# Performance work log

Measured on AMD Instinct MI355X. Metric: run time of the kernel, lower is better.

The kernel has to match this reference:

```python
import math
import jax, jax.numpy as jnp
import numpy as np

B, S, D, H = 4, 2048, 768, 8


def setup_inputs() -> dict:
    key = jax.random.key(0)
    ks = jax.random.split(key, 8)
    x = jax.random.normal(ks[0], (B, S, D), dtype=jnp.float32)
    # padding mask: True = masked position, shape [B, S, 1] as consumed by forward
    attention_mask = jax.random.randint(ks[1], (B, S, 1), 0, 2) == 1
    W_q = jax.random.normal(ks[2], (D, D), dtype=jnp.float32) * 0.02
    b_q = jax.random.normal(ks[3], (D,), dtype=jnp.float32) * 0.02
    W_v = jax.random.normal(ks[4], (D, D), dtype=jnp.float32) * 0.02
    b_v = jax.random.normal(ks[5], (D,), dtype=jnp.float32) * 0.02
    gamma = jnp.ones((D,), dtype=jnp.float32)
    beta = jnp.zeros((D,), dtype=jnp.float32)
    return {"x": x, "attention_mask": attention_mask, "W_q": W_q, "b_q": b_q,
            "W_v": W_v, "b_v": b_v, "gamma": gamma, "beta": beta}


def reference(x, attention_mask, W_q, b_q, W_v, b_v, gamma, beta):
    b, s, d = x.shape
    dk = d // H
    scale = math.sqrt(dk)
    q = (x @ W_q.T + b_q).reshape(b, s, H, dk).transpose(0, 2, 1, 3)  # [B,H,S,dk]
    # faithful to source: k and v BOTH use the V projection (original bug)
    kv = (x @ W_v.T + b_v).reshape(b, s, H, dk).transpose(0, 2, 1, 3)
    k = kv
    v = kv
    weight = jnp.einsum('bhid,bhjd->bhij', q, k) / scale  # [B,H,S,S]
    pad = attention_mask[:, None, :, :]                   # [B,1,S,1] -> broadcast over heads, j
    causal = jnp.triu(jnp.ones((s, s), dtype=bool), 1)    # [S,S]
    mask = pad | causal
    weight = jnp.where(mask, jnp.float32(-1e9), weight)
    # faithful: softmax over dim=2 (the query axis), as in the source
    score = jax.nn.softmax(weight, axis=2)
    out = jnp.einsum('bhij,bhjd->bhid', score, v)         # [B,H,S,dk]
    out = out.transpose(0, 2, 1, 3).reshape(b, s, d)
    out = out + x                                          # residual
    mu = jnp.mean(out, axis=-1, keepdims=True)
    var = jnp.mean((out - mu) ** 2, axis=-1, keepdims=True)
    return (out - mu) / jnp.sqrt(var + 1e-5) * gamma + beta
```

## Files before the change

### kernel.cpp

```cpp
#include <hip/hip_runtime.h>

#define B 4
#define S 2048
#define D 768
#define H 8
#define DK 96
#define NBH (B*H)
#define SD (B*S*D)

typedef __bf16 bf16x8 __attribute__((ext_vector_type(8)));
typedef float f32x4 __attribute__((ext_vector_type(4)));
typedef unsigned short ushort_t;
typedef __attribute__((ext_vector_type(8))) unsigned short ushort8;
typedef __attribute__((ext_vector_type(4))) unsigned short us4;

static constexpr float NEG = -1.0e9f;
static constexpr float SCALE_L2E = 0.14724515567714155f;

__device__ __forceinline__ float exp2v(float x) { return __builtin_amdgcn_exp2f(x); }

__device__ __forceinline__ ushort_t f2bf(float f) {
    union { float f; unsigned u; } v; v.f = f;
    unsigned r = v.u + 0x7fffu + ((v.u >> 16) & 1u);
    return (ushort_t)(r >> 16);
}

__device__ __forceinline__ unsigned cvt_pk(float a, float b) {
    unsigned d;
    asm("v_cvt_pk_bf16_f32 %0, %1, %2" : "=v"(d) : "v"(a), "v"(b));
    return d;
}
__device__ __forceinline__ ushort8 pack8(const float4& a, const float4& b) {
    union { unsigned u[4]; ushort8 s; } r;
    r.u[0] = cvt_pk(a.x, a.y); r.u[1] = cvt_pk(a.z, a.w);
    r.u[2] = cvt_pk(b.x, b.y); r.u[3] = cvt_pk(b.z, b.w);
    return r.s;
}
__device__ __forceinline__ us4 pack4(const float4& a) {
    union { unsigned u[2]; us4 s; } r;
    r.u[0] = cvt_pk(a.x, a.y); r.u[1] = cvt_pk(a.z, a.w);
    return r.s;
}

#define MFMA16(a, b, c) __builtin_amdgcn_mfma_f32_16x16x32_bf16((a), (b), (c), 0, 0, 0)

__global__ __launch_bounds__(256) void convert_bf16(
    const float* __restrict__ wq, const float* __restrict__ wv,
    ushort_t* __restrict__ wqb, ushort_t* __restrict__ wvb)
{
    const int stride = gridDim.x * 256;
    const int idx = blockIdx.x * 256 + threadIdx.x;
    for (int i = idx; i < (D * D) / 4; i += stride) {
        ((us4*)wqb)[i] = pack4(((const float4*)wq)[i]);
        ((us4*)wvb)[i] = pack4(((const float4*)wv)[i]);
    }
}

__global__ __launch_bounds__(256) void in_proj_gemm(
    const float* __restrict__ x,
    const ushort_t* __restrict__ wqb, const float* __restrict__ bq,
    const ushort_t* __restrict__ wvb, const float* __restrict__ bv,
    ushort_t* __restrict__ Qb, ushort_t* __restrict__ KVb,
    ushort_t* __restrict__ KVt)
{
    const ushort_t* __restrict__ Wm = blockIdx.z ? wvb : wqb;
    const float* __restrict__ bia   = blockIdx.z ? bv : bq;
    ushort_t* __restrict__ outp     = blockIdx.z ? KVb : Qb;
    const float osc = blockIdx.z ? 1.0f : SCALE_L2E;

    const int bn = blockIdx.x * 128;
    const int bm = blockIdx.y * 128;
    const int tid = threadIdx.x;
    const int lane = tid & 63;
    const int wid = tid >> 6;
    const int wm = (wid >> 1) * 64, wn = (wid & 1) * 64;
    const int lr = lane & 15, lg = lane >> 4;

    __shared__ __align__(16) ushort_t As[2][128][40];
    __shared__ __align__(16) ushort_t Bs[2][128][40];

    const int r0 = tid >> 2, c8 = (tid & 3) * 8;
    const float*    xg0 = &x [(size_t)(bm + r0) * D + c8];
    const float*    xg1 = xg0 + (size_t)64 * D;
    const ushort_t* wg0 = &Wm[(size_t)(bn + r0) * D + c8];
    const ushort_t* wg1 = wg0 + (size_t)64 * D;

    float4 xv[4];
    ushort8 wv2[2];

    f32x4 acc[4][4];
    #pragma unroll
    for (int m = 0; m < 4; ++m)
        #pragma unroll
        for (int n = 0; n < 4; ++n) acc[m][n] = (f32x4){0.f, 0.f, 0.f, 0.f};

    {
        xv[0] = *(const float4*)(xg0);     xv[1] = *(const float4*)(xg0 + 4);
        xv[2] = *(const float4*)(xg1);     xv[3] = *(const float4*)(xg1 + 4);
        wv2[0] = *(const ushort8*)(wg0);   wv2[1] = *(const ushort8*)(wg1);
        *(ushort8*)&As[0][r0][c8]      = pack8(xv[0], xv[1]);
        *(ushort8*)&As[0][r0 + 64][c8] = pack8(xv[2], xv[3]);
        *(ushort8*)&Bs[0][r0][c8]      = wv2[0];
        *(ushort8*)&Bs[0][r0 + 64][c8] = wv2[1];
    }

    for (int k = 0; k < 24; ++k) {
        __syncthreads();
        const int buf = k & 1;
        if (k < 23) {
            const int ko = (k + 1) * 32;
            xv[0] = *(const float4*)(xg0 + ko);     xv[1] = *(const float4*)(xg0 + ko + 4);
            xv[2] = *(const float4*)(xg1 + ko);     xv[3] = *(const float4*)(xg1 + ko + 4);
            wv2[0] = *(const ushort8*)(wg0 + ko);   wv2[1] = *(const ushort8*)(wg1 + ko);
        }
        bf16x8 a[4], bfr[4];
        #pragma unroll
        for (int m = 0; m < 4; ++m) a[m]   = *(const bf16x8*)&As[buf][wm + m * 16 + lr][lg * 8];
        #pragma unroll
        for (int n = 0; n < 4; ++n) bfr[n] = *(const bf16x8*)&Bs[buf][wn + n * 16 + lr][lg * 8];
        #pragma unroll
        for (int m = 0; m < 4; ++m)
            #pragma unroll
            for (int n = 0; n < 4; ++n)
                acc[m][n] = MFMA16(a[m], bfr[n], acc[m][n]);
        if (k < 23) {
            const int nb = (k + 1) & 1;
            *(ushort8*)&As[nb][r0][c8]      = pack8(xv[0], xv[1]);
            *(ushort8*)&As[nb][r0 + 64][c8] = pack8(xv[2], xv[3]);
            *(ushort8*)&Bs[nb][r0][c8]      = wv2[0];
            *(ushort8*)&Bs[nb][r0 + 64][c8] = wv2[1];
        }
    }

    #pragma unroll
    for (int m = 0; m < 4; ++m) {
        #pragma unroll
        for (int n = 0; n < 4; ++n) {
            int col = bn + wn + n * 16 + lr;
            float bb = bia[col];
            int row0 = bm + wm + m * 16 + lg * 4;
            us4 o;
            #pragma unroll
            for (int r = 0; r < 4; ++r) o[r] = f2bf((acc[m][n][r] + bb) * osc);
            #pragma unroll
            for (int r = 0; r < 4; ++r) outp[(size_t)(row0 + r) * D + col] = o[r];
            if (blockIdx.z) {
                int hh = col / DK, dd = col - hh * DK;
                int bb2 = row0 >> 11, ss = row0 & (S - 1);
                *(us4*)&KVt[((size_t)(bb2 * H + hh) * DK + dd) * S + ss] = o;
            }
        }
    }
}

__global__ __launch_bounds__(256) void col_stats(
    const ushort_t* __restrict__ Qb, const ushort_t* __restrict__ KVb,
    const int* __restrict__ amask,
    float* __restrict__ colM, float* __restrict__ colSinv)
{
    const int bh = blockIdx.y;
    const int jt = (blockIdx.x + 8 * ((bh >> 3) & 3)) & 31;
    const int b = bh >> 3, h = bh & 7;
    const int j0 = jt * 64;
    const int tid = threadIdx.x;
    const int lane = tid & 63;
    const int w = tid >> 6;
    const int lr = lane & 15, lg = lane >> 4;

    __shared__ __align__(16) ushort_t qs[2][64][104];
    __shared__ int pads[2][64];

    bf16x8 kf[3];
    #pragma unroll
    for (int ks2 = 0; ks2 < 3; ++ks2)
        kf[ks2] = *(const bf16x8*)&KVb[(size_t)(b * S + j0 + w * 16 + lr) * D + h * DK + ks2 * 32 + lg * 8];

    int kr[3], kc[3];
    const ushort_t* qg[3];
    #pragma unroll
    for (int k3 = 0; k3 < 3; ++k3) {
        int c = tid + k3 * 256;
        kr[k3] = c / 12; kc[k3] = (c % 12) * 8;
        qg[k3] = &Qb[(size_t)(b * S + j0 + kr[k3]) * D + h * DK + kc[k3]];
    }
    const int* pg = amask + b * S + j0 + (tid < 64 ? tid : 0);

    ushort8 pq[3]; int ppad = 0;
    #pragma unroll
    for (int k3 = 0; k3 < 3; ++k3) { pq[k3] = *(const ushort8*)qg[k3]; qg[k3] += (size_t)64 * D; }
    if (tid < 64) { ppad = *pg; }
    pg += 64;

    float m = NEG, ssum = 0.f;
    const int jg = j0 + w * 16 + lr;
    const int nit = (S / 64) - jt;

    for (int t = 0; t < nit; ++t) {
        const int buf = t & 1;
        const int i0 = j0 + t * 64;
        #pragma unroll
        for (int k3 = 0; k3 < 3; ++k3) *(ushort8*)&qs[buf][kr[k3]][kc[k3]] = pq[k3];
        if (tid < 64) pads[buf][tid] = ppad;
        __syncthreads();
        if (t + 1 < nit) {
            #pragma unroll
            for (int k3 = 0; k3 < 3; ++k3) { pq[k3] = *(const ushort8*)qg[k3]; qg[k3] += (size_t)64 * D; }
            if (tid < 64) { ppad = *pg; }
            pg += 64;
        }

        f32x4 dacc[4];
        #pragma unroll
        for (int f = 0; f < 4; ++f) dacc[f] = (f32x4){0.f, 0.f, 0.f, 0.f};
        #pragma unroll
        for (int ks2 = 0; ks2 < 3; ++ks2) {
            #pragma unroll
            for (int f = 0; f < 4; ++f) {
                bf16x8 afr = *(const bf16x8*)&qs[buf][f * 16 + lr][ks2 * 32 + lg * 8];
                dacc[f] = MFMA16(afr, kf[ks2], dacc[f]);
            }
        }

        #pragma unroll
        for (int f = 0; f < 4; ++f) {
            const int ib = f * 16 + lg * 4;
            float wv[4];
            #pragma unroll
            for (int r = 0; r < 4; ++r) {
                int ig = i0 + ib + r;
                wv[r] = (pads[buf][ib + r] != 0 || jg > ig) ? NEG : dacc[f][r];
            }
            float vmax = fmaxf(fmaxf(wv[0], wv[1]), fmaxf(wv[2], wv[3]));
            float mn = fmaxf(m, vmax);
            ssum = ssum * exp2v(m - mn)
                 + exp2v(wv[0] - mn) + exp2v(wv[1] - mn)
                 + exp2v(wv[2] - mn) + exp2v(wv[3] - mn);
            m = mn;
        }
    }

    float m2 = m, s2 = ssum;
    #pragma unroll
    for (int off = 16; off < 64; off <<= 1) {
        float mo = __shfl_xor(m2, off);
        float so = __shfl_xor(s2, off);
        float mn = fmaxf(m2, mo);
        s2 = s2 * exp2v(m2 - mn) + so * exp2v(mo - mn);
        m2 = mn;
    }
    if (lane < 16) {
        if (m2 == NEG) s2 += (float)j0;
        colM[bh * S + jg] = m2;
        colSinv[bh * S + jg] = 1.0f / s2;
    }
}

__global__ __launch_bounds__(256, 4) void attn_pv(
    const ushort_t* __restrict__ Qb, const ushort_t* __restrict__ KVb,
    const ushort_t* __restrict__ KVt,
    const int* __restrict__ amask,
    const float* __restrict__ colM, const float* __restrict__ colSinv,
    const float* __restrict__ x, float* __restrict__ out)
{
    const int bh = blockIdx.y;
    const int it = (blockIdx.x + 8 * ((bh >> 3) & 3)) & 31;
    const int b = bh >> 3, h = bh & 7;
    const int i0 = it * 64;
    const int tid = threadIdx.x;
    const int lane = tid & 63;
    const int w = tid >> 6;
    const int lr = lane & 15, lg = lane >> 4;

    __shared__ __align__(16) ushort_t kvs[64][104];
    __shared__ __align__(16) ushort_t kvt[96][88];
    __shared__ __align__(16) ushort_t ps[64][72];
    __shared__ __align__(16) float cm[64];
    __shared__ __align__(16) float csv[64];

    bf16x8 qf[3];
    #pragma unroll
    for (int ks2 = 0; ks2 < 3; ++ks2)
        qf[ks2] = *(const bf16x8*)&Qb[(size_t)(b * S + i0 + w * 16 + lr) * D + h * DK + ks2 * 32 + lg * 8];

    const int my_pad = (int)(amask[b * S + i0 + w * 16 + lr] != 0);
    const int i_g = i0 + w * 16 + lr;

    int kr[3], kc[3], tr[3], tc[3];
    const ushort_t* kvg[3];
    const ushort_t* ktg[3];
    #pragma unroll
    for (int k3 = 0; k3 < 3; ++k3) {
        int c = tid + k3 * 256;
        kr[k3] = c / 12;  kc[k3] = (c % 12) * 8;
        tr[k3] = c >> 3;  tc[k3] = (c & 7) * 8;
        kvg[k3] = &KVb[(size_t)(b * S + kr[k3]) * D + h * DK + kc[k3]];
        ktg[k3] = &KVt[((size_t)(b * H + h) * DK + tr[k3]) * S + tc[k3]];
    }
    const float* cmg  = colM    + (size_t)bh * S + (tid < 64 ? tid : 0);
    const float* csvg = colSinv + (size_t)bh * S + (tid < 64 ? tid : 0);

    ushort8 pkv[3], pkt[3]; float pcm = 0.f, pcsv = 0.f;
    #pragma unroll
    for (int k3 = 0; k3 < 3; ++k3) {
        pkv[k3] = *(const ushort8*)kvg[k3];  kvg[k3] += (size_t)64 * D;
        pkt[k3] = *(const ushort8*)ktg[k3];  ktg[k3] += 64;
    }
    if (tid < 64) { pcm = *cmg; pcsv = *csvg; }
    cmg += 64; csvg += 64;

    f32x4 acc[6];
    #pragma unroll
    for (int df = 0; df < 6; ++df) acc[df] = (f32x4){0.f, 0.f, 0.f, 0.f};

    for (int jt2 = 0; jt2 <= it; ++jt2) {
        const int j0 = jt2 * 64;
        __syncthreads();
        #pragma unroll
        for (int k3 = 0; k3 < 3; ++k3) {
            *(ushort8*)&kvs[kr[k3]][kc[k3]] = pkv[k3];
            *(ushort8*)&kvt[tr[k3]][tc[k3]] = pkt[k3];
        }
        if (tid < 64) { cm[tid] = pcm; csv[tid] = pcsv; }
        __syncthreads();
        if (jt2 < it) {
            #pragma unroll
            for (int k3 = 0; k3 < 3; ++k3) {
                pkv[k3] = *(const ushort8*)kvg[k3];  kvg[k3] += (size_t)64 * D;
                pkt[k3] = *(const ushort8*)ktg[k3];  ktg[k3] += 64;
            }
            if (tid < 64) { pcm = *cmg; pcsv = *csvg; }
            cmg += 64; csvg += 64;
        }

        f32x4 dacc[4];
        #pragma unroll
        for (int jf = 0; jf < 4; ++jf) dacc[jf] = (f32x4){0.f, 0.f, 0.f, 0.f};
        #pragma unroll
        for (int ks2 = 0; ks2 < 3; ++ks2) {
            #pragma unroll
            for (int jf = 0; jf < 4; ++jf) {
                bf16x8 bfr = *(const bf16x8*)&kvs[jf * 16 + lr][ks2 * 32 + lg * 8];
                dacc[jf] = MFMA16(bfr, qf[ks2], dacc[jf]);
            }
        }

        #pragma unroll
        for (int jf = 0; jf < 4; ++jf) {
            const int jbase = jf * 16 + lg * 4;
            f32x4 cmv  = *(const f32x4*)&cm[jbase];
            f32x4 csvv = *(const f32x4*)&csv[jbase];
            float pv[4];
            #pragma unroll
            for (int r = 0; r < 4; ++r) {
                int jgl = j0 + jbase + r;
                bool msk = my_pad || (jgl > i_g);
                float wvv = msk ? NEG : dacc[jf][r];
                pv[r] = exp2v(wvv - cmv[r]) * csvv[r];
            }
            union { unsigned u[2]; uint2 v; } o;
            o.u[0] = cvt_pk(pv[0], pv[1]);
            o.u[1] = cvt_pk(pv[2], pv[3]);
            *(uint2*)&ps[w * 16 + lr][jbase] = o.v;
        }

        #pragma unroll
        for (int ks2 = 0; ks2 < 2; ++ks2) {
            bf16x8 afr = *(const bf16x8*)&ps[w * 16 + lr][ks2 * 32 + lg * 8];
            #pragma unroll
            for (int df = 0; df < 6; ++df) {
                bf16x8 bfr = *(const bf16x8*)&kvt[df * 16 + lr][ks2 * 32 + lg * 8];
                acc[df] = MFMA16(afr, bfr, acc[df]);
            }
        }
    }

    #pragma unroll
    for (int df = 0; df < 6; ++df) {
        int d = h * DK + df * 16 + lr;
        #pragma unroll
        for (int r = 0; r < 4; ++r) {
            size_t gi = (size_t)(b * S + i0 + w * 16 + lg * 4 + r) * D + d;
            out[gi] = acc[df][r] + x[gi];
        }
    }
}

__global__ __launch_bounds__(256) void layer_norm(
    float* __restrict__ out,
    const float* __restrict__ gamma, const float* __restrict__ beta)
{
    const int row = blockIdx.x * 4 + (threadIdx.x >> 6);
    const int lane = threadIdx.x & 63;
    float* o = out + (size_t)row * D;

    float4 v[3];
    #pragma unroll
    for (int p = 0; p < 3; ++p) v[p] = *(const float4*)&o[lane * 4 + p * 256];

    float s = 0.f;
    #pragma unroll
    for (int p = 0; p < 3; ++p) s += v[p].x + v[p].y + v[p].z + v[p].w;
    #pragma unroll
    for (int off = 1; off < 64; off <<= 1) s += __shfl_xor(s, off);
    const float mu = s * (1.0f / D);

    float q = 0.f;
    #pragma unroll
    for (int p = 0; p < 3; ++p) {
        float a = v[p].x - mu, bb = v[p].y - mu, c = v[p].z - mu, dd = v[p].w - mu;
        q += a * a + bb * bb + c * c + dd * dd;
    }
    #pragma unroll
    for (int off = 1; off < 64; off <<= 1) q += __shfl_xor(q, off);
    const float inv = 1.0f / sqrtf(q * (1.0f / D) + 1e-5f);

    #pragma unroll
    for (int p = 0; p < 3; ++p) {
        float4 g = *(const float4*)&gamma[lane * 4 + p * 256];
        float4 bt = *(const float4*)&beta[lane * 4 + p * 256];
        float4 r;
        r.x = (v[p].x - mu) * inv * g.x + bt.x;
        r.y = (v[p].y - mu) * inv * g.y + bt.y;
        r.z = (v[p].z - mu) * inv * g.z + bt.z;
        r.w = (v[p].w - mu) * inv * g.w + bt.w;
        *(float4*)&o[lane * 4 + p * 256] = r;
    }
}

extern "C" void kernel_launch(void* const* d_in, const int* in_sizes, int n_in,
                              void* d_out, int out_size, void* d_ws, size_t ws_size,
                              hipStream_t stream)
{
    const float* x     = (const float*)d_in[0];
    const int*   amask = (const int*)  d_in[1];
    const float* Wq    = (const float*)d_in[2];
    const float* bq    = (const float*)d_in[3];
    const float* Wv    = (const float*)d_in[4];
    const float* bv    = (const float*)d_in[5];
    const float* gamma = (const float*)d_in[6];
    const float* beta  = (const float*)d_in[7];
    float* out = (float*)d_out;

    ushort_t* wqb  = (ushort_t*)d_ws;
    ushort_t* wvb  = wqb + (size_t)D * D;
    ushort_t* Qb   = wvb + (size_t)D * D;
    ushort_t* KVb  = Qb  + (size_t)SD;
    ushort_t* KVt  = KVb + (size_t)SD;
    float* colM    = (float*)(KVt + (size_t)SD);
    float* colSinv = colM + (size_t)NBH * S;

    convert_bf16<<<576, 256, 0, stream>>>(Wq, Wv, wqb, wvb);
    in_proj_gemm<<<dim3(D / 128, (B * S) / 128, 2), 256, 0, stream>>>(
        x, wqb, bq, wvb, bv, Qb, KVb, KVt);
    col_stats<<<dim3(S / 64, NBH), 256, 0, stream>>>(
        Qb, KVb, amask, colM, colSinv);
    attn_pv<<<dim3(S / 64, NBH), 256, 0, stream>>>(
        Qb, KVb, KVt, amask, colM, colSinv, x, out);
    layer_norm<<<(B * S) / 4, 256, 0, stream>>>(out, gamma, beta);
}
```

Measured before the change: 175.1 us.

## Double per-block tile to 128 rows in col_stats and attn_pv

Both attention kernels now give each block 128 columns or rows instead of 64, with each wave holding two 16-row fragments. Each staged Q or KV tile in shared memory is therefore reused for twice as many MFMAs, halving tile loads and block count. The tile-to-block mapping now reverses order for half the heads to balance causal work. The cost is more registers (launch bounds lowered to 3 waves), half as many blocks (512), and coarser load-balance granularity.

New measurement: 260.6 us. 48.9% more time.

```diff
diff --git a/kernel.cpp b/kernel.cpp
--- a/kernel.cpp
+++ b/kernel.cpp
@@ -153,15 +153,16 @@
     }
 }
 
-__global__ __launch_bounds__(256) void col_stats(
+__global__ __launch_bounds__(256, 3) void col_stats(
     const ushort_t* __restrict__ Qb, const ushort_t* __restrict__ KVb,
     const int* __restrict__ amask,
     float* __restrict__ colM, float* __restrict__ colSinv)
 {
     const int bh = blockIdx.y;
-    const int jt = (blockIdx.x + 8 * ((bh >> 3) & 3)) & 31;
+    const int bxs = blockIdx.x & 15;
+    const int jt = (bh & 16) ? (15 - bxs) : bxs;
     const int b = bh >> 3, h = bh & 7;
-    const int j0 = jt * 64;
+    const int j0 = jt * 128;
     const int tid = threadIdx.x;
     const int lane = tid & 63;
     const int w = tid >> 6;
@@ -170,10 +171,12 @@
     __shared__ __align__(16) ushort_t qs[2][64][104];
     __shared__ int pads[2][64];
 
-    bf16x8 kf[3];
-    #pragma unroll
-    for (int ks2 = 0; ks2 < 3; ++ks2)
-        kf[ks2] = *(const bf16x8*)&KVb[(size_t)(b * S + j0 + w * 16 + lr) * D + h * DK + ks2 * 32 + lg * 8];
+    bf16x8 kf[2][3];
+    #pragma unroll
+    for (int cf = 0; cf < 2; ++cf)
+        #pragma unroll
+        for (int ks2 = 0; ks2 < 3; ++ks2)
+            kf[cf][ks2] = *(const bf16x8*)&KVb[(size_t)(b * S + j0 + w * 32 + cf * 16 + lr) * D + h * DK + ks2 * 32 + lg * 8];
 
     int kr[3], kc[3];
     const ushort_t* qg[3];
@@ -191,9 +194,11 @@
     if (tid < 64) { ppad = *pg; }
     pg += 64;
 
-    float m = NEG, ssum = 0.f;
-    const int jg = j0 + w * 16 + lr;
-    const int nit = (S / 64) - jt;
+    float m[2] = {NEG, NEG}, ssum[2] = {0.f, 0.f};
+    int jg[2];
+    jg[0] = j0 + w * 32 + lr;
+    jg[1] = j0 + w * 32 + 16 + lr;
+    const int nit = 32 - 2 * jt;
 
     for (int t = 0; t < nit; ++t) {
         const int buf = t & 1;
@@ -209,53 +214,62 @@
             pg += 64;
         }
 
-        f32x4 dacc[4];
-        #pragma unroll
-        for (int f = 0; f < 4; ++f) dacc[f] = (f32x4){0.f, 0.f, 0.f, 0.f};
+        f32x4 dacc[2][4];
+        #pragma unroll
+        for (int cf = 0; cf < 2; ++cf)
+            #pragma unroll
+            for (int f = 0; f < 4; ++f) dacc[cf][f] = (f32x4){0.f, 0.f, 0.f, 0.f};
         #pragma unroll
         for (int ks2 = 0; ks2 < 3; ++ks2) {
             #pragma unroll
             for (int f = 0; f < 4; ++f) {
                 bf16x8 afr = *(const bf16x8*)&qs[buf][f * 16 + lr][ks2 * 32 + lg * 8];
-                dacc[f] = MFMA16(afr, kf[ks2], dacc[f]);
-            }
-        }
-
-        #pragma unroll
-        for (int f = 0; f < 4; ++f) {
-            const int ib = f * 16 + lg * 4;
-            float wv[4];
-            #pragma unroll
-            for (int r = 0; r < 4; ++r) {
-                int ig = i0 + ib + r;
-                wv[r] = (pads[buf][ib + r] != 0 || jg > ig) ? NEG : dacc[f][r];
-            }
-            float vmax = fmaxf(fmaxf(wv[0], wv[1]), fmaxf(wv[2], wv[3]));
-            float mn = fmaxf(m, vmax);
-            ssum = ssum * exp2v(m - mn)
-                 + exp2v(wv[0] - mn) + exp2v(wv[1] - mn)
-                 + exp2v(wv[2] - mn) + exp2v(wv[3] - mn);
-            m = mn;
-        }
-    }
-
-    float m2 = m, s2 = ssum;
-    #pragma unroll
-    for (int off = 16; off < 64; off <<= 1) {
-        float mo = __shfl_xor(m2, off);
-        float so = __shfl_xor(s2, off);
-        float mn = fmaxf(m2, mo);
-        s2 = s2 * exp2v(m2 - mn) + so * exp2v(mo - mn);
-        m2 = mn;
-    }
-    if (lane < 16) {
-        if (m2 == NEG) s2 += (float)j0;
-        colM[bh * S + jg] = m2;
-        colSinv[bh * S + jg] = 1.0f / s2;
-    }
-}
-
-__global__ __launch_bounds__(256, 4) void attn_pv(
+                dacc[0][f] = MFMA16(afr, kf[0][ks2], dacc[0][f]);
+                dacc[1][f] = MFMA16(afr, kf[1][ks2], dacc[1][f]);
+            }
+        }
+
+        #pragma unroll
+        for (int cf = 0; cf < 2; ++cf) {
+            #pragma unroll
+            for (int f = 0; f < 4; ++f) {
+                const int ib = f * 16 + lg * 4;
+                float wv[4];
+                #pragma unroll
+                for (int r = 0; r < 4; ++r) {
+                    int ig = i0 + ib + r;
+                    wv[r] = (pads[buf][ib + r] != 0 || jg[cf] > ig) ? NEG : dacc[cf][f][r];
+                }
+                float vmax = fmaxf(fmaxf(wv[0], wv[1]), fmaxf(wv[2], wv[3]));
+                float mn = fmaxf(m[cf], vmax);
+                ssum[cf] = ssum[cf] * exp2v(m[cf] - mn)
+                     + exp2v(wv[0] - mn) + exp2v(wv[1] - mn)
+                     + exp2v(wv[2] - mn) + exp2v(wv[3] - mn);
+                m[cf] = mn;
+            }
+        }
+    }
+
+    #pragma unroll
+    for (int cf = 0; cf < 2; ++cf) {
+        float m2 = m[cf], s2 = ssum[cf];
+        #pragma unroll
+        for (int off = 16; off < 64; off <<= 1) {
+            float mo = __shfl_xor(m2, off);
+            float so = __shfl_xor(s2, off);
+            float mn = fmaxf(m2, mo);
+            s2 = s2 * exp2v(m2 - mn) + so * exp2v(mo - mn);
+            m2 = mn;
+        }
+        if (lane < 16) {
+            if (m2 == NEG) s2 += (float)j0;
+            colM[bh * S + j0 + w * 32 + cf * 16 + lane] = m2;
+            colSinv[bh * S + j0 + w * 32 + cf * 16 + lane] = 1.0f / s2;
+        }
+    }
+}
+
+__global__ __launch_bounds__(256, 3) void attn_pv(
     const ushort_t* __restrict__ Qb, const ushort_t* __restrict__ KVb,
     const ushort_t* __restrict__ KVt,
     const int* __restrict__ amask,
@@ -263,27 +277,32 @@
     const float* __restrict__ x, float* __restrict__ out)
 {
     const int bh = blockIdx.y;
-    const int it = (blockIdx.x + 8 * ((bh >> 3) & 3)) & 31;
+    const int bxs = blockIdx.x & 15;
+    const int it = (bh & 16) ? (15 - bxs) : bxs;
     const int b = bh >> 3, h = bh & 7;
-    const int i0 = it * 64;
+    const int i0 = it * 128;
     const int tid = threadIdx.x;
     const int lane = tid & 63;
     const int w = tid >> 6;
     const int lr = lane & 15, lg = lane >> 4;
 
     __shared__ __align__(16) ushort_t kvs[64][104];
-    __shared__ __align__(16) ushort_t kvt[96][88];
-    __shared__ __align__(16) ushort_t ps[64][72];
+    __shared__ __align__(16) ushort_t kvt[96][72];
+    __shared__ __align__(16) ushort_t ps[128][72];
     __shared__ __align__(16) float cm[64];
     __shared__ __align__(16) float csv[64];
 
-    bf16x8 qf[3];
-    #pragma unroll
-    for (int ks2 = 0; ks2 < 3; ++ks2)
-        qf[ks2] = *(const bf16x8*)&Qb[(size_t)(b * S + i0 + w * 16 + lr) * D + h * DK + ks2 * 32 + lg * 8];
-
-    const int my_pad = (int)(amask[b * S + i0 + w * 16 + lr] != 0);
-    const int i_g = i0 + w * 16 + lr;
+    bf16x8 qf[2][3];
+    int my_pad[2], i_g[2];
+    #pragma unroll
+    for (int rf = 0; rf < 2; ++rf) {
+        const int row = i0 + w * 32 + rf * 16 + lr;
+        #pragma unroll
+        for (int ks2 = 0; ks2 < 3; ++ks2)
+            qf[rf][ks2] = *(const bf16x8*)&Qb[(size_t)(b * S + row) * D + h * DK + ks2 * 32 + lg * 8];
+        my_pad[rf] = (int)(amask[b * S + row] != 0);
+        i_g[rf] = row;
+    }
 
     int kr[3], kc[3], tr[3], tc[3];
     const ushort_t* kvg[3];
@@ -308,11 +327,14 @@
     if (tid < 64) { pcm = *cmg; pcsv = *csvg; }
     cmg += 64; csvg += 64;
 
-    f32x4 acc[6];
-    #pragma unroll
-    for (int df = 0; df < 6; ++df) acc[df] = (f32x4){0.f, 0.f, 0.f, 0.f};
-
-    for (int jt2 = 0; jt2 <= it; ++jt2) {
+    f32x4 acc[2][6];
+    #pragma unroll
+    for (int rf = 0; rf < 2; ++rf)
+        #pragma unroll
+        for (int df = 0; df < 6; ++df) acc[rf][df] = (f32x4){0.f, 0.f, 0.f, 0.f};
+
+    const int nj = 2 * it + 2;
+    for (int jt2 = 0; jt2 < nj; ++jt2) {
         const int j0 = jt2 * 64;
         __syncthreads();
         #pragma unroll
@@ -322,7 +344,7 @@
         }
         if (tid < 64) { cm[tid] = pcm; csv[tid] = pcsv; }
         __syncthreads();
-        if (jt2 < it) {
+        if (jt2 + 1 < nj) {
             #pragma unroll
             for (int k3 = 0; k3 < 3; ++k3) {
                 pkv[k3] = *(const ushort8*)kvg[k3];  kvg[k3] += (size_t)64 * D;
@@ -332,55 +354,66 @@
             cmg += 64; csvg += 64;
         }
 
-        f32x4 dacc[4];
-        #pragma unroll
-        for (int jf = 0; jf < 4; ++jf) dacc[jf] = (f32x4){0.f, 0.f, 0.f, 0.f};
+        f32x4 dacc[2][4];
+        #pragma unroll
+        for (int rf = 0; rf < 2; ++rf)
+            #pragma unroll
+            for (int jf = 0; jf < 4; ++jf) dacc[rf][jf] = (f32x4){0.f, 0.f, 0.f, 0.f};
         #pragma unroll
         for (int ks2 = 0; ks2 < 3; ++ks2) {
             #pragma unroll
             for (int jf = 0; jf < 4; ++jf) {
                 bf16x8 bfr = *(const bf16x8*)&kvs[jf * 16 + lr][ks2 * 32 + lg * 8];
-                dacc[jf] = MFMA16(bfr, qf[ks2], dacc[jf]);
-            }
-        }
-
-        #pragma unroll
-        for (int jf = 0; jf < 4; ++jf) {
-            const int jbase = jf * 16 + lg * 4;
-            f32x4 cmv  = *(const f32x4*)&cm[jbase];
-            f32x4 csvv = *(const f32x4*)&csv[jbase];
-            float pv[4];
-            #pragma unroll
-            for (int r = 0; r < 4; ++r) {
-                int jgl = j0 + jbase + r;
-                bool msk = my_pad || (jgl > i_g);
-                float wvv = msk ? NEG : dacc[jf][r];
-                pv[r] = exp2v(wvv - cmv[r]) * csvv[r];
-            }
-            union { unsigned u[2]; uint2 v; } o;
-            o.u[0] = cvt_pk(pv[0], pv[1]);
-            o.u[1] = cvt_pk(pv[2], pv[3]);
-            *(uint2*)&ps[w * 16 + lr][jbase] = o.v;
+                dacc[0][jf] = MFMA16(bfr, qf[0][ks2], dacc[0][jf]);
+                dacc[1][jf] = MFMA16(bfr, qf[1][ks2], dacc[1][jf]);
+            }
+        }
+
+        #pragma unroll
+        for (int rf = 0; rf < 2; ++rf) {
+            #pragma unroll
+            for (int jf = 0; jf < 4; ++jf) {
+                const int jbase = jf * 16 + lg * 4;
+                f32x4 cmv  = *(const f32x4*)&cm[jbase];
+                f32x4 csvv = *(const f32x4*)&csv[jbase];
+                float pv[4];
+                #pragma unroll
+                for (int r = 0; r < 4; ++r) {
+                    int jgl = j0 + jbase + r;
+                    bool msk = my_pad[rf] || (jgl > i_g[rf]);
+                    float wvv = msk ? NEG : dacc[rf][jf][r];
+                    pv[r] = exp2v(wvv - cmv[r]) * csvv[r];
+                }
+                union { unsigned u[2]; uint2 v; } o;
+                o.u[0] = cvt_pk(pv[0], pv[1]);
+                o.u[1] = cvt_pk(pv[2], pv[3]);
+                *(uint2*)&ps[w * 32 + rf * 16 + lr][jbase] = o.v;
+            }
         }
 
         #pragma unroll
         for (int ks2 = 0; ks2 < 2; ++ks2) {
-            bf16x8 afr = *(const bf16x8*)&ps[w * 16 + lr][ks2 * 32 + lg * 8];
+            bf16x8 afr0 = *(const bf16x8*)&ps[w * 32 + lr][ks2 * 32 + lg * 8];
+            bf16x8 afr1 = *(const bf16x8*)&ps[w * 32 + 16 + lr][ks2 * 32 + lg * 8];
             #pragma unroll
             for (int df = 0; df < 6; ++df) {
                 bf16x8 bfr = *(const bf16x8*)&kvt[df * 16 + lr][ks2 * 32 + lg * 8];
-                acc[df] = MFMA16(afr, bfr, acc[df]);
-            }
-        }
-    }
-
-    #pragma unroll
-    for (int df = 0; df < 6; ++df) {
-        int d = h * DK + df * 16 + lr;
-        #pragma unroll
-        for (int r = 0; r < 4; ++r) {
-            size_t gi = (size_t)(b * S + i0 + w * 16 + lg * 4 + r) * D + d;
-            out[gi] = acc[df][r] + x[gi];
+                acc[0][df] = MFMA16(afr0, bfr, acc[0][df]);
+                acc[1][df] = MFMA16(afr1, bfr, acc[1][df]);
+            }
+        }
+    }
+
+    #pragma unroll
+    for (int rf = 0; rf < 2; ++rf) {
+        #pragma unroll
+        for (int df = 0; df < 6; ++df) {
+            int d = h * DK + df * 16 + lr;
+            #pragma unroll
+            for (int r = 0; r < 4; ++r) {
+                size_t gi = (size_t)(b * S + i0 + w * 32 + rf * 16 + lg * 4 + r) * D + d;
+                out[gi] = acc[rf][df][r] + x[gi];
+            }
         }
     }
 }
@@ -452,9 +485,9 @@
     convert_bf16<<<576, 256, 0, stream>>>(Wq, Wv, wqb, wvb);
     in_proj_gemm<<<dim3(D / 128, (B * S) / 128, 2), 256, 0, stream>>>(
         x, wqb, bq, wvb, bv, Qb, KVb, KVt);
-    col_stats<<<dim3(S / 64, NBH), 256, 0, stream>>>(
+    col_stats<<<dim3(16, NBH), 256, 0, stream>>>(
         Qb, KVb, amask, colM, colSinv);
-    attn_pv<<<dim3(S / 64, NBH), 256, 0, stream>>>(
+    attn_pv<<<dim3(16, NBH), 256, 0, stream>>>(
         Qb, KVb, KVt, amask, colM, colSinv, x, out);
     layer_norm<<<(B * S) / 4, 256, 0, stream>>>(out, gamma, beta);
 }
```
